# Kernel optimization log

Measured on AMD Instinct MI355X. Metric: run time of the kernel, lower is better.

The kernel has to match this reference:

```python
import jax, jax.numpy as jnp
import numpy as np

B, NQ, NKV, D, H = 2, 2048, 2048, 1024, 16
DH = D // H
EPS = 1e-5


def _ln(x, g, b):
    mu = jnp.mean(x, axis=-1, keepdims=True)
    var = jnp.mean(jnp.square(x - mu), axis=-1, keepdims=True)
    return (x - mu) * jax.lax.rsqrt(var + EPS) * g + b


def setup_inputs() -> dict:
    key = jax.random.key(0)
    ks = jax.random.split(key, 16)
    s = 0.02
    return {
        "X": jax.random.normal(ks[0], (B, NQ, D), jnp.float32),
        "Y": jax.random.normal(ks[1], (B, NKV, D), jnp.float32),
        "Wq": jax.random.normal(ks[2], (D, D), jnp.float32) * s,
        "bq": jnp.zeros((D,), jnp.float32),
        "Wk": jax.random.normal(ks[3], (D, D), jnp.float32) * s,
        "bk": jnp.zeros((D,), jnp.float32),
        "Wv": jax.random.normal(ks[4], (D, D), jnp.float32) * s,
        "bv": jnp.zeros((D,), jnp.float32),
        "null_k": jax.random.normal(ks[5], (1, 1, D), jnp.float32) * s,
        "g0": jnp.ones((D,), jnp.float32),
        "b0": jnp.zeros((D,), jnp.float32),
        "g0kv": jnp.ones((D,), jnp.float32),
        "b0kv": jnp.zeros((D,), jnp.float32),
        "g1": jnp.ones((D,), jnp.float32),
        "b1": jnp.zeros((D,), jnp.float32),
        "W1": jax.random.normal(ks[6], (D, 4 * D), jnp.float32) * s,
        "bf1": jnp.zeros((4 * D,), jnp.float32),
        "W2": jax.random.normal(ks[7], (4 * D, D), jnp.float32) * s,
        "bf2": jnp.zeros((D,), jnp.float32),
    }


def reference(X, Y, Wq, bq, Wk, bk, Wv, bv, null_k, g0, b0, g0kv, b0kv,
              g1, b1, W1, bf1, W2, bf2):
    # pre-layer-norm on Q-side and KV-side inputs
    Xn = _ln(X, g0, b0)
    Yn = _ln(Y, g0kv, b0kv)
    Q = Xn @ Wq + bq                       # [B, NQ, D]
    K = Yn @ Wk + bk                       # [B, NKV, D]
    V = Yn @ Wv + bv
    # null KV: learned null key, zero value appended along seq dim
    K = jnp.concatenate([K, jnp.broadcast_to(null_k, (B, 1, D))], axis=1)   # [B, NKV+1, D]
    V = jnp.concatenate([V, jnp.zeros((B, 1, D), V.dtype)], axis=1)
    # split heads (split along feature dim == reshape to (.., H, DH))
    Qh = Q.reshape(B, NQ, H, DH)
    Kh = K.reshape(B, NKV + 1, H, DH)
    Vh = V.reshape(B, NKV + 1, H, DH)
    # scores scaled by 1/sqrt(dim_KV) (NOT head dim), softmax_temp == 1.0
    A = jnp.einsum('bqhd,bkhd->bhqk', Qh, Kh) / jnp.sqrt(jnp.float32(D))
    A = jax.nn.softmax(A, axis=-1)          # [B, H, NQ, NKV+1]
    O = jnp.einsum('bhqk,bkhd->bqhd', A, Vh).reshape(B, NQ, D)
    # no head mixing (fc_mix_heads=None); residual uses identity fc_res
    Hres = O + X
    Hr = _ln(Hres, g1, b1)
    ff = jax.nn.gelu(Hr @ W1 + bf1, approximate=False) @ W2 + bf2
    return Hres + ff
```

## Files before the change

kernel.cpp:

```cpp
#include <hip/hip_runtime.h>
#include <hip/hip_bf16.h>
#include <math.h>
#include <stdint.h>

typedef __bf16 bf16x8 __attribute__((ext_vector_type(8)));
typedef __bf16 bf16x4 __attribute__((ext_vector_type(4)));
typedef float floatx4 __attribute__((ext_vector_type(4)));
typedef short shortx4 __attribute__((ext_vector_type(4)));
typedef unsigned int uint32x2 __attribute__((ext_vector_type(2)));

#define NQS   2048
#define NKVS  2048
#define NKV1  2049
#define DM    1024
#define NH    16
#define DHD   64
#define BATCH 2
#define ROWS  (BATCH * NQS)

__device__ __forceinline__ void gld_lds16(const __bf16* gp, __bf16* lp) {
    __builtin_amdgcn_global_load_lds(
        (const __attribute__((address_space(1))) uint32_t*)(uintptr_t)gp,
        (__attribute__((address_space(3))) uint32_t*)(uintptr_t)lp,
        16, 0, 0);
}

__device__ __forceinline__ float gelu_fast(float x) {
    const float u = x * x;
    const float e = __builtin_amdgcn_exp2f(x * (-2.3022077f + (-0.1029431f) * u));
    return x * __builtin_amdgcn_rcpf(1.0f + e);
}

__global__ __launch_bounds__(256) void ln2_to_bf16(
    const float* __restrict__ X, const float* __restrict__ Y,
    const float* __restrict__ g0, const float* __restrict__ b0,
    const float* __restrict__ g0kv, const float* __restrict__ b0kv,
    __bf16* __restrict__ Xn, __bf16* __restrict__ Yn)
{
    int row = blockIdx.x;
    const float *src, *gamma, *beta; __bf16* dst;
    if (row < ROWS) { src = X; gamma = g0; beta = b0; dst = Xn; }
    else { row -= ROWS; src = Y; gamma = g0kv; beta = b0kv; dst = Yn; }
    const int tid = threadIdx.x;
    const float4 v = ((const float4*)(src + (size_t)row * DM))[tid];
    float s  = v.x + v.y + v.z + v.w;
    float sq = v.x * v.x + v.y * v.y + v.z * v.z + v.w * v.w;
    for (int off = 1; off < 64; off <<= 1) {
        s  += __shfl_xor(s, off);
        sq += __shfl_xor(sq, off);
    }
    __shared__ float red[8];
    const int wave = tid >> 6, lane = tid & 63;
    if (lane == 0) { red[wave * 2] = s; red[wave * 2 + 1] = sq; }
    __syncthreads();
    s  = red[0] + red[2] + red[4] + red[6];
    sq = red[1] + red[3] + red[5] + red[7];
    const float mu  = s * (1.0f / DM);
    const float var = sq * (1.0f / DM) - mu * mu;
    const float rs  = rsqrtf(var + 1e-5f);
    const float4 gv = ((const float4*)gamma)[tid];
    const float4 bv = ((const float4*)beta)[tid];
    bf16x4 o;
    o[0] = (__bf16)((v.x - mu) * rs * gv.x + bv.x);
    o[1] = (__bf16)((v.y - mu) * rs * gv.y + bv.y);
    o[2] = (__bf16)((v.z - mu) * rs * gv.z + bv.z);
    o[3] = (__bf16)((v.w - mu) * rs * gv.w + bv.w);
    *(bf16x4*)(dst + (size_t)row * DM + tid * 4) = o;
}

__global__ __launch_bounds__(256) void resid_ln(
    const float* __restrict__ X, const __bf16* __restrict__ O,
    const float* __restrict__ gamma, const float* __restrict__ beta,
    float* __restrict__ Hres, __bf16* __restrict__ Hr)
{
    const int row = blockIdx.x;
    const int tid = threadIdx.x;
    const float4 xv = ((const float4*)(X + (size_t)row * DM))[tid];
    const bf16x4 ov = *(const bf16x4*)(O + (size_t)row * DM + tid * 4);
    float4 v;
    v.x = xv.x + (float)ov[0];
    v.y = xv.y + (float)ov[1];
    v.z = xv.z + (float)ov[2];
    v.w = xv.w + (float)ov[3];
    ((float4*)(Hres + (size_t)row * DM))[tid] = v;

    float s  = v.x + v.y + v.z + v.w;
    float sq = v.x * v.x + v.y * v.y + v.z * v.z + v.w * v.w;
    for (int off = 1; off < 64; off <<= 1) {
        s  += __shfl_xor(s, off);
        sq += __shfl_xor(sq, off);
    }
    __shared__ float red[8];
    const int wave = tid >> 6, lane = tid & 63;
    if (lane == 0) { red[wave * 2] = s; red[wave * 2 + 1] = sq; }
    __syncthreads();
    s  = red[0] + red[2] + red[4] + red[6];
    sq = red[1] + red[3] + red[5] + red[7];
    const float mu  = s * (1.0f / DM);
    const float var = sq * (1.0f / DM) - mu * mu;
    const float rs  = rsqrtf(var + 1e-5f);
    const float4 gv = ((const float4*)gamma)[tid];
    const float4 bv = ((const float4*)beta)[tid];
    bf16x4 o;
    o[0] = (__bf16)((v.x - mu) * rs * gv.x + bv.x);
    o[1] = (__bf16)((v.y - mu) * rs * gv.y + bv.y);
    o[2] = (__bf16)((v.z - mu) * rs * gv.z + bv.z);
    o[3] = (__bf16)((v.w - mu) * rs * gv.w + bv.w);
    *(bf16x4*)(Hr + (size_t)row * DM + tid * 4) = o;
}

__global__ __launch_bounds__(256) void transpose3_f32_bf16(
    const float* __restrict__ Wq, const float* __restrict__ Wk,
    const float* __restrict__ Wv, __bf16* __restrict__ WqT,
    __bf16* __restrict__ WkT, __bf16* __restrict__ WvT)
{
    __shared__ float tile[32][33];
    const int z = blockIdx.z;
    const float* in = (z == 0) ? Wq : (z == 1) ? Wk : Wv;
    __bf16* out = (z == 0) ? WqT : (z == 1) ? WkT : WvT;
    const int c0 = blockIdx.x * 32, r0 = blockIdx.y * 32;
    const int tx = threadIdx.x, ty = threadIdx.y;
#pragma unroll
    for (int i = 0; i < 4; i++)
        tile[ty + i * 8][tx] = in[(size_t)(r0 + ty + i * 8) * DM + c0 + tx];
    __syncthreads();
#pragma unroll
    for (int i = 0; i < 4; i++)
        out[(size_t)(c0 + ty + i * 8) * DM + r0 + tx] = (__bf16)tile[tx][ty + i * 8];
}

__global__ __launch_bounds__(256) void transpose_ffw(
    const float* __restrict__ W1, const float* __restrict__ W2,
    __bf16* __restrict__ W1T, __bf16* __restrict__ W2T)
{
    __shared__ float tile[32][33];
    const int z = blockIdx.z;
    const float* in; __bf16* out; int R, C, c0, r0;
    if (z == 0) { in = W1; out = W1T; R = DM; C = 4 * DM; c0 = blockIdx.x * 32; r0 = blockIdx.y * 32; }
    else        { in = W2; out = W2T; R = 4 * DM; C = DM; c0 = blockIdx.y * 32; r0 = blockIdx.x * 32; }
    const int tx = threadIdx.x, ty = threadIdx.y;
#pragma unroll
    for (int i = 0; i < 4; i++)
        tile[ty + i * 8][tx] = in[(size_t)(r0 + ty + i * 8) * C + c0 + tx];
    __syncthreads();
#pragma unroll
    for (int i = 0; i < 4; i++)
        out[(size_t)(c0 + ty + i * 8) * R + r0 + tx] = (__bf16)tile[tx][ty + i * 8];
}

__global__ __launch_bounds__(256) void fill_null(
    const float* __restrict__ null_k, __bf16* __restrict__ Kb,
    __bf16* __restrict__ Vt)
{
    const int i = blockIdx.x * 256 + threadIdx.x;
    if (i < BATCH * DM) {
        const int b = i >> 10, d = i & (DM - 1);
        Kb[((size_t)b * NKV1 + NKVS) * DM + d] = (__bf16)null_k[d];
    }
    if (i < BATCH * NH * DHD * 8) {
        const int bhd = i >> 3, kvp = i & 7;
        Vt[(size_t)bhd * 2056 + 2048 + kvp] = (__bf16)0.0f;
    }
}

template<int MODE, int ACT>
__global__ __launch_bounds__(256) void gemm_bt(
    const __bf16* __restrict__ A, const __bf16* __restrict__ Bt,
    const float* __restrict__ bias, void* __restrict__ outp,
    const float* __restrict__ resid, int M, int N, int K)
{
    __shared__ __bf16 As[128][32];
    __shared__ __bf16 Bs[128][32];
    const int tid  = threadIdx.x;
    const int lane = tid & 63, wave = tid >> 6;
    const int g = lane >> 4, c = lane & 15;
    const int m0 = blockIdx.y * 128, n0 = blockIdx.x * 128;
    const int wm = (wave >> 1) * 64, wn = (wave & 1) * 64;

    floatx4 acc[4][4] = {};

    const int srow = tid >> 2;
    const int schk = (tid & 3) * 8;
    const __bf16* Ag = A  + (size_t)(m0 + srow) * K + schk;
    const __bf16* Bg = Bt + (size_t)(n0 + srow) * K + schk;
    __bf16* lA0 = &As[srow][schk];
    __bf16* lA1 = &As[srow + 64][schk];
    __bf16* lB0 = &Bs[srow][schk];
    __bf16* lB1 = &Bs[srow + 64][schk];

    int kbeg = 0, kend = K;
    if (MODE == 4) { const int KS = K >> 2; kbeg = blockIdx.z * KS; kend = kbeg + KS; }

    for (int k0 = kbeg; k0 < kend; k0 += 32) {
        __syncthreads();
        gld_lds16(Ag + k0, lA0);
        gld_lds16(Ag + (size_t)64 * K + k0, lA1);
        gld_lds16(Bg + k0, lB0);
        gld_lds16(Bg + (size_t)64 * K + k0, lB1);
        __syncthreads();
        bf16x8 af[4], bfr[4];
#pragma unroll
        for (int i = 0; i < 4; i++) af[i]  = *(const bf16x8*)&As[wm + i * 16 + c][g * 8];
#pragma unroll
        for (int j = 0; j < 4; j++) bfr[j] = *(const bf16x8*)&Bs[wn + j * 16 + c][g * 8];
#pragma unroll
        for (int i = 0; i < 4; i++)
#pragma unroll
            for (int j = 0; j < 4; j++)
                acc[i][j] = __builtin_amdgcn_mfma_f32_16x16x32_bf16(af[i], bfr[j], acc[i][j], 0, 0, 0);
    }

    __bf16* obf = (__bf16*)outp;
    float*  of  = (float*)outp;
#pragma unroll
    for (int i = 0; i < 4; i++) {
#pragma unroll
        for (int j = 0; j < 4; j++) {
            const int row = m0 + wm + i * 16 + g * 4;
            const int col = n0 + wn + j * 16 + c;
            const float bb = (MODE == 4) ? 0.0f : bias[col];
            float xs[4];
#pragma unroll
            for (int r = 0; r < 4; r++) {
                float x = acc[i][j][r] + bb;
                if (ACT == 1) x = gelu_fast(x);
                xs[r] = x;
            }
            if (MODE == 0) {
#pragma unroll
                for (int r = 0; r < 4; r++)
                    obf[(size_t)(row + r) * N + col] = (__bf16)xs[r];
            } else if (MODE == 4) {
#pragma unroll
                for (int r = 0; r < 4; r++)
                    of[((size_t)blockIdx.z * M + row + r) * N + col] = xs[r];
            }
        }
    }
}

__global__ __launch_bounds__(256) void qkv_gemm(
    const __bf16* __restrict__ Xn, const __bf16* __restrict__ Yn,
    const __bf16* __restrict__ WqT, const __bf16* __restrict__ WkT,
    const __bf16* __restrict__ WvT,
    const float* __restrict__ bq, const float* __restrict__ bk,
    const float* __restrict__ bv,
    __bf16* __restrict__ Qbf, __bf16* __restrict__ Kbf,
    __bf16* __restrict__ Vt)
{
    __shared__ __bf16 As[128][32];
    __shared__ __bf16 Bs[128][32];
    const int z = blockIdx.z;
    const __bf16* A    = (z == 0) ? Xn  : Yn;
    const __bf16* Bt   = (z == 0) ? WqT : (z == 1) ? WkT : WvT;
    const float*  bias = (z == 0) ? bq  : (z == 1) ? bk  : bv;

    const int tid  = threadIdx.x;
    const int lane = tid & 63, wave = tid >> 6;
    const int g = lane >> 4, c = lane & 15;
    const int m0 = blockIdx.y * 128, n0 = blockIdx.x * 128;
    const int wm = (wave >> 1) * 64, wn = (wave & 1) * 64;

    floatx4 acc[4][4] = {};

    const int srow = tid >> 2;
    const int schk = (tid & 3) * 8;
    const __bf16* Ag = A  + (size_t)(m0 + srow) * DM + schk;
    const __bf16* Bg = Bt + (size_t)(n0 + srow) * DM + schk;
    __bf16* lA0 = &As[srow][schk];
    __bf16* lA1 = &As[srow + 64][schk];
    __bf16* lB0 = &Bs[srow][schk];
    __bf16* lB1 = &Bs[srow + 64][schk];

    for (int k0 = 0; k0 < DM; k0 += 32) {
        __syncthreads();
        gld_lds16(Ag + k0, lA0);
        gld_lds16(Ag + (size_t)64 * DM + k0, lA1);
        gld_lds16(Bg + k0, lB0);
        gld_lds16(Bg + (size_t)64 * DM + k0, lB1);
        __syncthreads();
        bf16x8 af[4], bfr[4];
#pragma unroll
        for (int i = 0; i < 4; i++) af[i]  = *(const bf16x8*)&As[wm + i * 16 + c][g * 8];
#pragma unroll
        for (int j = 0; j < 4; j++) bfr[j] = *(const bf16x8*)&Bs[wn + j * 16 + c][g * 8];
#pragma unroll
        for (int i = 0; i < 4; i++)
#pragma unroll
            for (int j = 0; j < 4; j++)
                acc[i][j] = __builtin_amdgcn_mfma_f32_16x16x32_bf16(af[i], bfr[j], acc[i][j], 0, 0, 0);
    }

#pragma unroll
    for (int i = 0; i < 4; i++) {
#pragma unroll
        for (int j = 0; j < 4; j++) {
            const int row = m0 + wm + i * 16 + g * 4;
            const int col = n0 + wn + j * 16 + c;
            const float bb = bias[col];
            float xs[4];
#pragma unroll
            for (int r = 0; r < 4; r++) xs[r] = acc[i][j][r] + bb;
            if (z == 0) {
#pragma unroll
                for (int r = 0; r < 4; r++)
                    Qbf[(size_t)(row + r) * DM + col] = (__bf16)xs[r];
            } else if (z == 1) {
#pragma unroll
                for (int r = 0; r < 4; r++) {
                    const int rr = row + r;
                    Kbf[(size_t)(rr + (rr >> 11)) * DM + col] = (__bf16)xs[r];
                }
            } else {
                const int b  = row >> 11;
                const int kv = row & 2047;
                const size_t base =
                    ((size_t)((b * NH + (col >> 6)) * DHD + (col & 63))) * 2056 + kv;
                bf16x4 pk;
                pk[0] = (__bf16)xs[0]; pk[1] = (__bf16)xs[1];
                pk[2] = (__bf16)xs[2]; pk[3] = (__bf16)xs[3];
                *(bf16x4*)(Vt + base) = pk;
            }
        }
    }
}

__global__ __launch_bounds__(256) void ff2_reduce(
    const float* __restrict__ part, const float* __restrict__ bias,
    const float* __restrict__ Hres, float* __restrict__ out)
{
    const size_t f4 = (size_t)blockIdx.x * 256 + threadIdx.x;
    const int c4 = (int)(f4 & (DM / 4 - 1));
    const size_t stride4 = (size_t)ROWS * DM / 4;
    float4 a = ((const float4*)part)[f4];
    const float4 p1 = ((const float4*)part)[f4 + stride4];
    const float4 p2 = ((const float4*)part)[f4 + 2 * stride4];
    const float4 p3 = ((const float4*)part)[f4 + 3 * stride4];
    const float4 b  = ((const float4*)bias)[c4];
    const float4 hr = ((const float4*)Hres)[f4];
    a.x += p1.x + p2.x + p3.x + b.x + hr.x;
    a.y += p1.y + p2.y + p3.y + b.y + hr.y;
    a.z += p1.z + p2.z + p3.z + b.z + hr.z;
    a.w += p1.w + p2.w + p3.w + b.w + hr.w;
    ((float4*)out)[f4] = a;
}

__global__ __launch_bounds__(256, 4) void attn_kernel(
    const __bf16* __restrict__ Q, const __bf16* __restrict__ Kb,
    const __bf16* __restrict__ Vt, __bf16* __restrict__ O)
{
    __shared__ __bf16 Ks[2][64][72];
    __shared__ __bf16 Vs[2][64][72];

    const int tid = threadIdx.x, lane = tid & 63, w = tid >> 6;
    const int g = lane >> 4, c = lane & 15;
    const int h = blockIdx.y, b = blockIdx.z;
    const int q0w = blockIdx.x * 64 + w * 16;

    const float QSC = 0.03125f * 1.44269504088896f;
    bf16x8 qf[2];
    const __bf16* Qbase = Q + ((size_t)(b * NQS + q0w + c)) * DM + h * DHD;
    qf[0] = *(const bf16x8*)(Qbase + g * 8);
    qf[1] = *(const bf16x8*)(Qbase + 32 + g * 8);
#pragma unroll
    for (int e = 0; e < 8; e++) {
        qf[0][e] = (__bf16)((float)qf[0][e] * QSC);
        qf[1][e] = (__bf16)((float)qf[1][e] * QSC);
    }

    floatx4 lacc = {};
    floatx4 oacc[4] = {};

    const int kr = tid >> 3, kch = (tid & 7) * 8;
    const int vd = tid >> 2, vch = (tid & 3) * 8;
    const __bf16* Kb_base = Kb + (size_t)b * NKV1 * DM + h * DHD + kch;
    const __bf16* Vt_base = Vt + ((size_t)(b * NH + h) * DHD + vd) * 2056 + vch;
    const uint4 zero4 = make_uint4(0u, 0u, 0u, 0u);

    uint4 pk0, pk1, pv0, pv1;

    auto load_full = [&](int kv0) {
        pk0 = *(const uint4*)(Kb_base + (size_t)(kv0 + kr) * DM);
        pk1 = *(const uint4*)(Kb_base + (size_t)(kv0 + kr + 32) * DM);
        pv0 = *(const uint4*)(Vt_base + kv0);
        pv1 = *(const uint4*)(Vt_base + kv0 + 32);
    };
    auto load_tail = [&](int kv0) {
        const int kv1 = kv0 + kr, kv2 = kv1 + 32;
        pk0 = (kv1 < NKV1) ? *(const uint4*)(Kb_base + (size_t)kv1 * DM) : zero4;
        pk1 = (kv2 < NKV1) ? *(const uint4*)(Kb_base + (size_t)kv2 * DM) : zero4;
        pv0 = (kv0 + vch + 7  < 2056) ? *(const uint4*)(Vt_base + kv0)      : zero4;
        pv1 = (kv0 + vch + 39 < 2056) ? *(const uint4*)(Vt_base + kv0 + 32) : zero4;
    };
    auto store_buf = [&](int p) {
        *(uint4*)&Ks[p][kr][kch]      = pk0;
        *(uint4*)&Ks[p][kr + 32][kch] = pk1;
        *(uint4*)&Vs[p][vd][vch]      = pv0;
        *(uint4*)&Vs[p][vd][vch + 32] = pv1;
    };
    auto compute = [&](int p, int kv0, bool tail) {
        floatx4 s[4];
#pragma unroll
        for (int kvt = 0; kvt < 4; kvt++)
#pragma unroll
            for (int r = 0; r < 4; r++) s[kvt][r] = -6.0f;
        bf16x8 kf[4][2];
#pragma unroll
        for (int kvt = 0; kvt < 4; kvt++) {
            kf[kvt][0] = *(const bf16x8*)&Ks[p][kvt * 16 + c][g * 8];
            kf[kvt][1] = *(const bf16x8*)&Ks[p][kvt * 16 + c][32 + g * 8];
        }
#pragma unroll
        for (int kvt = 0; kvt < 4; kvt++) {
            s[kvt] = __builtin_amdgcn_mfma_f32_16x16x32_bf16(kf[kvt][0], qf[0], s[kvt], 0, 0, 0);
            s[kvt] = __builtin_amdgcn_mfma_f32_16x16x32_bf16(kf[kvt][1], qf[1], s[kvt], 0, 0, 0);
        }

        if (tail) {
#pragma unroll
            for (int kvt = 0; kvt < 4; kvt++)
#pragma unroll
                for (int r = 0; r < 4; r++)
                    if (kv0 + kvt * 16 + g * 4 + r >= NKV1) s[kvt][r] = -1e30f;
        }

        shortx4 pf[4];
#pragma unroll
        for (int kvt = 0; kvt < 4; kvt++) {
            float p0 = __builtin_amdgcn_exp2f(s[kvt][0]);
            float p1 = __builtin_amdgcn_exp2f(s[kvt][1]);
            float p2 = __builtin_amdgcn_exp2f(s[kvt][2]);
            float p3 = __builtin_amdgcn_exp2f(s[kvt][3]);
            lacc[0] += p0; lacc[1] += p1; lacc[2] += p2; lacc[3] += p3;
            uint32x2 pk;
            pk[0] = (__builtin_bit_cast(unsigned int, p0) >> 16) |
                    (__builtin_bit_cast(unsigned int, p1) & 0xFFFF0000u);
            pk[1] = (__builtin_bit_cast(unsigned int, p2) >> 16) |
                    (__builtin_bit_cast(unsigned int, p3) & 0xFFFF0000u);
            pf[kvt] = __builtin_bit_cast(shortx4, pk);
        }

#pragma unroll
        for (int kvt = 0; kvt < 4; kvt++) {
            shortx4 vfr[4];
#pragma unroll
            for (int dt = 0; dt < 4; dt++)
                vfr[dt] = *(const shortx4*)&Vs[p][dt * 16 + c][kvt * 16 + g * 4];
#pragma unroll
            for (int dt = 0; dt < 4; dt++)
                oacc[dt] = __builtin_amdgcn_mfma_f32_16x16x16bf16_1k(
                    vfr[dt], pf[kvt], oacc[dt], 0, 0, 0);
        }
    };

    load_full(0);
    store_buf(0);
    __syncthreads();
    for (int it = 0; it < 32; it++) {
        const int p = it & 1;
        if (it < 31) load_full((it + 1) * 64);
        else         load_tail(2048);
        compute(p, it * 64, false);
        store_buf(p ^ 1);
        __syncthreads();
    }
    compute(0, 2048, true);

    float l = lacc[0] + lacc[1] + lacc[2] + lacc[3];
    l += __shfl_xor(l, 16);
    l += __shfl_xor(l, 32);
    const float inv_l = 1.0f / l;

    __bf16* Ob = O + ((size_t)(b * NQS + q0w + c)) * DM + h * DHD;
#pragma unroll
    for (int dt = 0; dt < 4; dt++) {
        bf16x4 ob;
#pragma unroll
        for (int r = 0; r < 4; r++) ob[r] = (__bf16)(oacc[dt][r] * inv_l);
        *(bf16x4*)(Ob + dt * 16 + g * 4) = ob;
    }
}

extern "C" void kernel_launch(void* const* d_in, const int* in_sizes, int n_in,
                              void* d_out, int out_size, void* d_ws, size_t ws_size,
                              hipStream_t stream)
{
    const float* X      = (const float*)d_in[0];
    const float* Y      = (const float*)d_in[1];
    const float* Wq     = (const float*)d_in[2];
    const float* bq     = (const float*)d_in[3];
    const float* Wk     = (const float*)d_in[4];
    const float* bk     = (const float*)d_in[5];
    const float* Wv     = (const float*)d_in[6];
    const float* bv     = (const float*)d_in[7];
    const float* null_k = (const float*)d_in[8];
    const float* g0     = (const float*)d_in[9];
    const float* b0     = (const float*)d_in[10];
    const float* g0kv   = (const float*)d_in[11];
    const float* b0kv   = (const float*)d_in[12];
    const float* g1     = (const float*)d_in[13];
    const float* b1     = (const float*)d_in[14];
    const float* W1     = (const float*)d_in[15];
    const float* bf1    = (const float*)d_in[16];
    const float* W2     = (const float*)d_in[17];
    const float* bf2    = (const float*)d_in[18];
    float* out = (float*)d_out;

    char* p = (char*)d_ws;
    __bf16* W2T  = (__bf16*)p; p += (size_t)4 * DM * DM * 2;
    float*  Hres = (float*)p;  p += (size_t)ROWS * DM * 4;
    __bf16* Gbf  = (__bf16*)p; p += (size_t)ROWS * 4 * DM * 2;
    char* scratch = p;
    __bf16* Xn   = (__bf16*)p; p += (size_t)ROWS * DM * 2;
    __bf16* Yn   = (__bf16*)p; p += (size_t)ROWS * DM * 2;
    __bf16* WqT  = (__bf16*)p; p += (size_t)DM * DM * 2;
    __bf16* WkT  = (__bf16*)p; p += (size_t)DM * DM * 2;
    __bf16* WvT  = (__bf16*)p; p += (size_t)DM * DM * 2;
    __bf16* W1T  = (__bf16*)p; p += (size_t)4 * DM * DM * 2;
    __bf16* Qbf  = (__bf16*)p; p += (size_t)ROWS * DM * 2;
    __bf16* Kbf  = (__bf16*)p; p += (size_t)BATCH * NKV1 * DM * 2;
    __bf16* Vt   = (__bf16*)p; p += (size_t)BATCH * NH * DHD * 2056 * 2;
    __bf16* Obf  = (__bf16*)p; p += (size_t)ROWS * DM * 2;
    __bf16* Hr   = (__bf16*)p; p += (size_t)ROWS * DM * 2;
    float* Part  = (float*)scratch;

    ln2_to_bf16<<<2 * ROWS, 256, 0, stream>>>(X, Y, g0, b0, g0kv, b0kv, Xn, Yn);

    transpose3_f32_bf16<<<dim3(DM / 32, DM / 32, 3), dim3(32, 8), 0, stream>>>(
        Wq, Wk, Wv, WqT, WkT, WvT);
    transpose_ffw<<<dim3(128, 32, 2), dim3(32, 8), 0, stream>>>(W1, W2, W1T, W2T);

    qkv_gemm<<<dim3(DM / 128, ROWS / 128, 3), 256, 0, stream>>>(
        Xn, Yn, WqT, WkT, WvT, bq, bk, bv, Qbf, Kbf, Vt);
    fill_null<<<64, 256, 0, stream>>>(null_k, Kbf, Vt);

    attn_kernel<<<dim3(NQS / 64, NH, BATCH), 256, 0, stream>>>(Qbf, Kbf, Vt, Obf);

    resid_ln<<<ROWS, 256, 0, stream>>>(X, Obf, g1, b1, Hres, Hr);

    gemm_bt<0, 1><<<dim3(4 * DM / 128, ROWS / 128), 256, 0, stream>>>(
        Hr, W1T, bf1, (void*)Gbf, nullptr, ROWS, 4 * DM, DM);
    gemm_bt<4, 0><<<dim3(DM / 128, ROWS / 128, 4), 256, 0, stream>>>(
        Gbf, W2T, bf2, (void*)Part, nullptr, ROWS, DM, 4 * DM);
    ff2_reduce<<<ROWS * DM / 1024, 256, 0, stream>>>(Part, bf2, Hres, out);
}
```

Measured before the change: 408.8 us.

## Restructure attention kernel: 32 queries per wave, async LDS loads, swizzle, remapped grid

Each wave now handles two 16-row query tiles, so every K/V fragment read from shared memory feeds twice as many MFMAs. Register-staged K/V copies are replaced by direct global-to-LDS loads into unpadded buffers, with an XOR swizzle to avoid bank conflicts. MFMA sections are wrapped in s_setprio, and a 1D grid of 512 blocks is remapped so that blocks sharing a head and batch are grouped together for L2 locality. In exchange, register pressure doubles (launch bounds drop to 2), and there are fewer, larger blocks, which may reduce occupancy and latency hiding.

Result: faster. 390.1 us (-4.6%).

```diff
diff --git a/kernel.cpp b/kernel.cpp
--- a/kernel.cpp
+++ b/kernel.cpp
@@ -345,139 +345,161 @@
     ((float4*)out)[f4] = a;
 }
 
-__global__ __launch_bounds__(256, 4) void attn_kernel(
+__global__ __launch_bounds__(256, 2) void attn_kernel(
     const __bf16* __restrict__ Q, const __bf16* __restrict__ Kb,
     const __bf16* __restrict__ Vt, __bf16* __restrict__ O)
 {
-    __shared__ __bf16 Ks[2][64][72];
-    __shared__ __bf16 Vs[2][64][72];
+    __shared__ __bf16 Ks[2][64][64];
+    __shared__ __bf16 Vs[2][64][64];
 
     const int tid = threadIdx.x, lane = tid & 63, w = tid >> 6;
     const int g = lane >> 4, c = lane & 15;
-    const int h = blockIdx.y, b = blockIdx.z;
-    const int q0w = blockIdx.x * 64 + w * 16;
+
+    const int hw   = blockIdx.x;
+    const int slot = hw >> 3;
+    const int hb   = (hw & 7) | ((slot >> 4) << 3);
+    const int h = hb & 15, b = hb >> 4;
+    const int q0w = (slot & 15) * 128 + w * 32;
 
     const float QSC = 0.03125f * 1.44269504088896f;
-    bf16x8 qf[2];
-    const __bf16* Qbase = Q + ((size_t)(b * NQS + q0w + c)) * DM + h * DHD;
-    qf[0] = *(const bf16x8*)(Qbase + g * 8);
-    qf[1] = *(const bf16x8*)(Qbase + 32 + g * 8);
-#pragma unroll
-    for (int e = 0; e < 8; e++) {
-        qf[0][e] = (__bf16)((float)qf[0][e] * QSC);
-        qf[1][e] = (__bf16)((float)qf[1][e] * QSC);
-    }
-
-    floatx4 lacc = {};
-    floatx4 oacc[4] = {};
-
-    const int kr = tid >> 3, kch = (tid & 7) * 8;
-    const int vd = tid >> 2, vch = (tid & 3) * 8;
-    const __bf16* Kb_base = Kb + (size_t)b * NKV1 * DM + h * DHD + kch;
-    const __bf16* Vt_base = Vt + ((size_t)(b * NH + h) * DHD + vd) * 2056 + vch;
-    const uint4 zero4 = make_uint4(0u, 0u, 0u, 0u);
-
-    uint4 pk0, pk1, pv0, pv1;
-
-    auto load_full = [&](int kv0) {
-        pk0 = *(const uint4*)(Kb_base + (size_t)(kv0 + kr) * DM);
-        pk1 = *(const uint4*)(Kb_base + (size_t)(kv0 + kr + 32) * DM);
-        pv0 = *(const uint4*)(Vt_base + kv0);
-        pv1 = *(const uint4*)(Vt_base + kv0 + 32);
+    bf16x8 qf[2][2];
+#pragma unroll
+    for (int qt = 0; qt < 2; qt++) {
+        const __bf16* Qbase = Q + ((size_t)(b * NQS + q0w + qt * 16 + c)) * DM + h * DHD;
+        qf[qt][0] = *(const bf16x8*)(Qbase + g * 8);
+        qf[qt][1] = *(const bf16x8*)(Qbase + 32 + g * 8);
+#pragma unroll
+        for (int e = 0; e < 8; e++) {
+            qf[qt][0][e] = (__bf16)((float)qf[qt][0][e] * QSC);
+            qf[qt][1][e] = (__bf16)((float)qf[qt][1][e] * QSC);
+        }
+    }
+
+    floatx4 lacc[2] = {};
+    floatx4 oacc[2][4] = {};
+
+    const int srow = tid >> 3;
+    const int schk = (tid & 7) ^ (srow & 7);
+    const __bf16* Kg  = Kb + (size_t)b * NKV1 * DM + h * DHD + schk * 8;
+    const __bf16* Vg  = Vt + ((size_t)(b * NH + h) * DHD + srow) * 2056;
+    const __bf16* Vg2 = Vg + (size_t)32 * 2056;
+    const int vcol0 = schk * 8;
+
+    auto stage = [&](int p, int kv0, bool tail) {
+        __bf16* kd0 = &Ks[p][0][0]  + tid * 8;
+        __bf16* kd1 = &Ks[p][32][0] + tid * 8;
+        __bf16* vd0 = &Vs[p][0][0]  + tid * 8;
+        __bf16* vd1 = &Vs[p][32][0] + tid * 8;
+        if (!tail) {
+            gld_lds16(Kg + (size_t)(kv0 + srow) * DM, kd0);
+            gld_lds16(Kg + (size_t)(kv0 + srow + 32) * DM, kd1);
+            gld_lds16(Vg + kv0 + vcol0, vd0);
+            gld_lds16(Vg2 + kv0 + vcol0, vd1);
+        } else {
+            const int r0 = min(kv0 + srow, NKVS);
+            const int r1 = min(kv0 + srow + 32, NKVS);
+            const int vc = min(kv0 + vcol0, NKVS);
+            gld_lds16(Kg + (size_t)r0 * DM, kd0);
+            gld_lds16(Kg + (size_t)r1 * DM, kd1);
+            gld_lds16(Vg + vc, vd0);
+            gld_lds16(Vg2 + vc, vd1);
+        }
     };
-    auto load_tail = [&](int kv0) {
-        const int kv1 = kv0 + kr, kv2 = kv1 + 32;
-        pk0 = (kv1 < NKV1) ? *(const uint4*)(Kb_base + (size_t)kv1 * DM) : zero4;
-        pk1 = (kv2 < NKV1) ? *(const uint4*)(Kb_base + (size_t)kv2 * DM) : zero4;
-        pv0 = (kv0 + vch + 7  < 2056) ? *(const uint4*)(Vt_base + kv0)      : zero4;
-        pv1 = (kv0 + vch + 39 < 2056) ? *(const uint4*)(Vt_base + kv0 + 32) : zero4;
-    };
-    auto store_buf = [&](int p) {
-        *(uint4*)&Ks[p][kr][kch]      = pk0;
-        *(uint4*)&Ks[p][kr + 32][kch] = pk1;
-        *(uint4*)&Vs[p][vd][vch]      = pv0;
-        *(uint4*)&Vs[p][vd][vch + 32] = pv1;
-    };
+
     auto compute = [&](int p, int kv0, bool tail) {
-        floatx4 s[4];
-#pragma unroll
-        for (int kvt = 0; kvt < 4; kvt++)
-#pragma unroll
-            for (int r = 0; r < 4; r++) s[kvt][r] = -6.0f;
-        bf16x8 kf[4][2];
+        floatx4 s[2][4];
+#pragma unroll
+        for (int qt = 0; qt < 2; qt++)
+#pragma unroll
+            for (int kvt = 0; kvt < 4; kvt++)
+#pragma unroll
+                for (int r = 0; r < 4; r++) s[qt][kvt][r] = -6.0f;
+
+        const int sw = c & 7;
+        __builtin_amdgcn_s_setprio(1);
 #pragma unroll
         for (int kvt = 0; kvt < 4; kvt++) {
-            kf[kvt][0] = *(const bf16x8*)&Ks[p][kvt * 16 + c][g * 8];
-            kf[kvt][1] = *(const bf16x8*)&Ks[p][kvt * 16 + c][32 + g * 8];
-        }
-#pragma unroll
-        for (int kvt = 0; kvt < 4; kvt++) {
-            s[kvt] = __builtin_amdgcn_mfma_f32_16x16x32_bf16(kf[kvt][0], qf[0], s[kvt], 0, 0, 0);
-            s[kvt] = __builtin_amdgcn_mfma_f32_16x16x32_bf16(kf[kvt][1], qf[1], s[kvt], 0, 0, 0);
-        }
+            const bf16x8 kf0 = *(const bf16x8*)&Ks[p][kvt * 16 + c][(g ^ sw) * 8];
+            const bf16x8 kf1 = *(const bf16x8*)&Ks[p][kvt * 16 + c][((4 | g) ^ sw) * 8];
+#pragma unroll
+            for (int qt = 0; qt < 2; qt++) {
+                s[qt][kvt] = __builtin_amdgcn_mfma_f32_16x16x32_bf16(kf0, qf[qt][0], s[qt][kvt], 0, 0, 0);
+                s[qt][kvt] = __builtin_amdgcn_mfma_f32_16x16x32_bf16(kf1, qf[qt][1], s[qt][kvt], 0, 0, 0);
+            }
+        }
+        __builtin_amdgcn_s_setprio(0);
 
         if (tail) {
 #pragma unroll
-            for (int kvt = 0; kvt < 4; kvt++)
-#pragma unroll
-                for (int r = 0; r < 4; r++)
-                    if (kv0 + kvt * 16 + g * 4 + r >= NKV1) s[kvt][r] = -1e30f;
-        }
-
-        shortx4 pf[4];
-#pragma unroll
-        for (int kvt = 0; kvt < 4; kvt++) {
-            float p0 = __builtin_amdgcn_exp2f(s[kvt][0]);
-            float p1 = __builtin_amdgcn_exp2f(s[kvt][1]);
-            float p2 = __builtin_amdgcn_exp2f(s[kvt][2]);
-            float p3 = __builtin_amdgcn_exp2f(s[kvt][3]);
-            lacc[0] += p0; lacc[1] += p1; lacc[2] += p2; lacc[3] += p3;
-            uint32x2 pk;
-            pk[0] = (__builtin_bit_cast(unsigned int, p0) >> 16) |
-                    (__builtin_bit_cast(unsigned int, p1) & 0xFFFF0000u);
-            pk[1] = (__builtin_bit_cast(unsigned int, p2) >> 16) |
-                    (__builtin_bit_cast(unsigned int, p3) & 0xFFFF0000u);
-            pf[kvt] = __builtin_bit_cast(shortx4, pk);
-        }
-
+            for (int qt = 0; qt < 2; qt++)
+#pragma unroll
+                for (int kvt = 0; kvt < 4; kvt++)
+#pragma unroll
+                    for (int r = 0; r < 4; r++)
+                        if (kv0 + kvt * 16 + g * 4 + r >= NKV1) s[qt][kvt][r] = -1e30f;
+        }
+
+        shortx4 pf[2][4];
+#pragma unroll
+        for (int qt = 0; qt < 2; qt++)
+#pragma unroll
+            for (int kvt = 0; kvt < 4; kvt++) {
+                float p0 = __builtin_amdgcn_exp2f(s[qt][kvt][0]);
+                float p1 = __builtin_amdgcn_exp2f(s[qt][kvt][1]);
+                float p2 = __builtin_amdgcn_exp2f(s[qt][kvt][2]);
+                float p3 = __builtin_amdgcn_exp2f(s[qt][kvt][3]);
+                lacc[qt][0] += p0; lacc[qt][1] += p1;
+                lacc[qt][2] += p2; lacc[qt][3] += p3;
+                uint32x2 pk;
+                pk[0] = (__builtin_bit_cast(unsigned int, p0) >> 16) |
+                        (__builtin_bit_cast(unsigned int, p1) & 0xFFFF0000u);
+                pk[1] = (__builtin_bit_cast(unsigned int, p2) >> 16) |
+                        (__builtin_bit_cast(unsigned int, p3) & 0xFFFF0000u);
+                pf[qt][kvt] = __builtin_bit_cast(shortx4, pk);
+            }
+
+        __builtin_amdgcn_s_setprio(1);
 #pragma unroll
         for (int kvt = 0; kvt < 4; kvt++) {
             shortx4 vfr[4];
 #pragma unroll
+            for (int dt = 0; dt < 4; dt++) {
+                const int slotp = (kvt * 2 + (g >> 1)) ^ sw;
+                vfr[dt] = *(const shortx4*)&Vs[p][dt * 16 + c][slotp * 8 + (g & 1) * 4];
+            }
+#pragma unroll
             for (int dt = 0; dt < 4; dt++)
-                vfr[dt] = *(const shortx4*)&Vs[p][dt * 16 + c][kvt * 16 + g * 4];
-#pragma unroll
-            for (int dt = 0; dt < 4; dt++)
-                oacc[dt] = __builtin_amdgcn_mfma_f32_16x16x16bf16_1k(
-                    vfr[dt], pf[kvt], oacc[dt], 0, 0, 0);
-        }
+#pragma unroll
+                for (int qt = 0; qt < 2; qt++)
+                    oacc[qt][dt] = __builtin_amdgcn_mfma_f32_16x16x16bf16_1k(
+                        vfr[dt], pf[qt][kvt], oacc[qt][dt], 0, 0, 0);
+        }
+        __builtin_amdgcn_s_setprio(0);
     };
 
-    load_full(0);
-    store_buf(0);
+    stage(0, 0, false);
     __syncthreads();
     for (int it = 0; it < 32; it++) {
-        const int p = it & 1;
-        if (it < 31) load_full((it + 1) * 64);
-        else         load_tail(2048);
-        compute(p, it * 64, false);
-        store_buf(p ^ 1);
+        stage((it + 1) & 1, (it + 1) * 64, it == 31);
+        compute(it & 1, it * 64, false);
         __syncthreads();
     }
     compute(0, 2048, true);
 
-    float l = lacc[0] + lacc[1] + lacc[2] + lacc[3];
-    l += __shfl_xor(l, 16);
-    l += __shfl_xor(l, 32);
-    const float inv_l = 1.0f / l;
-
-    __bf16* Ob = O + ((size_t)(b * NQS + q0w + c)) * DM + h * DHD;
-#pragma unroll
-    for (int dt = 0; dt < 4; dt++) {
-        bf16x4 ob;
-#pragma unroll
-        for (int r = 0; r < 4; r++) ob[r] = (__bf16)(oacc[dt][r] * inv_l);
-        *(bf16x4*)(Ob + dt * 16 + g * 4) = ob;
+#pragma unroll
+    for (int qt = 0; qt < 2; qt++) {
+        float l = lacc[qt][0] + lacc[qt][1] + lacc[qt][2] + lacc[qt][3];
+        l += __shfl_xor(l, 16);
+        l += __shfl_xor(l, 32);
+        const float inv_l = 1.0f / l;
+        __bf16* Ob = O + ((size_t)(b * NQS + q0w + qt * 16 + c)) * DM + h * DHD;
+#pragma unroll
+        for (int dt = 0; dt < 4; dt++) {
+            bf16x4 ob;
+#pragma unroll
+            for (int r = 0; r < 4; r++) ob[r] = (__bf16)(oacc[qt][dt][r] * inv_l);
+            *(bf16x4*)(Ob + dt * 16 + g * 4) = ob;
+        }
     }
 }
 
@@ -534,7 +556,7 @@
         Xn, Yn, WqT, WkT, WvT, bq, bk, bv, Qbf, Kbf, Vt);
     fill_null<<<64, 256, 0, stream>>>(null_k, Kbf, Vt);
 
-    attn_kernel<<<dim3(NQS / 64, NH, BATCH), 256, 0, stream>>>(Qbf, Kbf, Vt, Obf);
+    attn_kernel<<<dim3(512), 256, 0, stream>>>(Qbf, Kbf, Vt, Obf);
 
     resid_ln<<<ROWS, 256, 0, stream>>>(X, Obf, g1, b1, Hres, Hr);
 
```
